# Optimization experiments

Hardware: AMD Instinct MI355X
Metric: run time of the kernel (lower is better)

Reference implementation:

```python
import jax, jax.numpy as jnp
import numpy as np

N = 1024       # nodes
D1 = 64        # hidden_dim_1
D2 = 64        # hidden_dim_2
E = 16384      # edges
P = 8192       # query pairs
MAXX = 100     # max node label -> Embedding(MAXX+1, D1)
EPS = 1e-5     # LayerNorm eps (no affine)


def _ln(t):
    m = jnp.mean(t, axis=-1, keepdims=True)
    v = jnp.mean((t - m) ** 2, axis=-1, keepdims=True)
    return (t - m) / jnp.sqrt(v + EPS)


def setup_inputs() -> dict:
    key = jax.random.key(0)
    ks = jax.random.split(key, 12)
    s = 0.1
    x = jax.random.randint(ks[0], (N,), 0, MAXX + 1)
    ei = jax.random.randint(ks[1], (2, E), 0, N)
    pos = jax.random.randint(ks[2], (P, 2), 0, N)
    emb = jax.random.normal(ks[3], (MAXX + 1, D1)) * s
    sage_Wl = jax.random.normal(ks[4], (2, D1, D1)) * s   # lin_l weight (aggr path, has bias)
    sage_bl = jnp.zeros((2, D1))
    sage_Wr = jax.random.normal(ks[5], (2, D1, D1)) * s   # lin_r weight (root path, no bias)
    h_W = jax.random.normal(ks[6], (D1 + 1, D2)) * s
    h_b = jnp.zeros((D2,))
    g_W = jax.random.normal(ks[7], (D1 + 1 + 2 * D2, D2)) * s
    g_b = jnp.zeros((D2,))
    lin_W = jax.random.normal(ks[8], (D2, 1)) * s
    lin_b = jnp.zeros((1,))
    return {"x": x, "ei": ei, "pos": pos, "emb": emb,
            "sage_Wl": sage_Wl, "sage_bl": sage_bl, "sage_Wr": sage_Wr,
            "h_W": h_W, "h_b": h_b, "g_W": g_W, "g_b": g_b,
            "lin_W": lin_W, "lin_b": lin_b}


def reference(x, ei, pos, emb, sage_Wl, sage_bl, sage_Wr, h_W, h_b, g_W, g_b, lin_W, lin_b):
    n = N
    src, dst = ei[0], ei[1]
    h = emb[x]                                            # (n, D1)
    # SAGEConv x2: mean-aggregate src->dst, lin_l(aggr)+bias + lin_r(root); then LN (no affine, no relu)
    deg = jax.ops.segment_sum(jnp.ones((E,), h.dtype), dst, num_segments=n)
    deg = jnp.maximum(deg, 1.0)[:, None]
    for i in range(2):
        aggr = jax.ops.segment_sum(h[src], dst, num_segments=n) / deg
        h = _ln(aggr @ sage_Wl[i] + sage_bl[i] + h @ sage_Wr[i])
    # pairwise outer product features: (n, n, D1)
    A = h[:, None, :] * h[None, :, :]
    eim = jnp.zeros((n * n,), h.dtype).at[src * n + dst].set(1.0).reshape(n, n, 1)
    A = jnp.concatenate([A, eim], axis=-1)                # (n, n, D1+1)
    # mataggr: B = h_1(A); row/col sums; D = cat(A, vec_p, vec_q); g_1(D)
    B = jax.nn.relu(_ln(A @ h_W + h_b))                   # (n, n, D2)
    vec_p = jnp.sum(B, axis=1, keepdims=True)             # (n, 1, D2)
    vec_q = jnp.sum(B, axis=0, keepdims=True)             # (1, n, D2)
    Dm = jnp.concatenate([A,
                          jnp.broadcast_to(vec_p, (n, n, D2)),
                          jnp.broadcast_to(vec_q, (n, n, D2))], axis=-1)
    G = jax.nn.relu(_ln(Dm @ g_W + g_b))                  # (n, n, D2)
    # symmetrize and gather query pairs
    S = (G * jnp.transpose(G, (1, 0, 2))).reshape(n * n, D2)
    sel = S[pos[:, 0] * n + pos[:, 1]]                    # (P, D2)
    return sel @ lin_W + lin_b                            # (P, 1)
```

## Files before the change

kernel.cpp:

```cpp
#include <hip/hip_runtime.h>
#include <hip/hip_bf16.h>

#define NN 1024
#define DD 64
#define EE 16384
#define PP 8192
#define EPSF 1e-5f
#define SWP (DD + 8)
#define NBC 64

typedef __hip_bfloat16 bf16;
typedef __attribute__((ext_vector_type(8))) short short8;
typedef __attribute__((ext_vector_type(4))) float f32x4;

static __device__ __forceinline__ float dec1(const void* src, int i, int fl) {
    if (fl) return ((const float*)src)[i];
    return __bfloat162float(((const bf16*)src)[i]);
}
static __device__ __forceinline__ unsigned short f2bf_u(float f) {
    bf16 h = __float2bfloat16(f);
    return *reinterpret_cast<unsigned short*>(&h);
}
static __device__ __forceinline__ float bfu2f(unsigned short u) {
    return __uint_as_float(((unsigned int)u) << 16);
}
static __device__ __forceinline__ int probe_fl(const void* emb) {
    int lane = threadIdx.x & 63;
    unsigned short raw = ((const unsigned short*)emb)[lane];
    float v = __uint_as_float(((unsigned int)raw) << 16);
    return (__ballot(!(fabsf(v) <= 1e3f)) != 0ull) ? 1 : 0;
}

__global__ __launch_bounds__(1024) void k_prep(
        const void* __restrict__ emb, const void* __restrict__ sWl,
        const void* __restrict__ sbl, const void* __restrict__ sWr,
        const void* __restrict__ hW, const void* __restrict__ hb,
        const void* __restrict__ gW, const void* __restrict__ gb,
        const void* __restrict__ lW, const void* __restrict__ lb,
        const int* __restrict__ x, const int* __restrict__ ei,
        float* __restrict__ Wlf, float* __restrict__ blf, float* __restrict__ Wrf,
        float* __restrict__ WfT, float* __restrict__ hbw,
        float* __restrict__ gWf, float* __restrict__ linf,
        unsigned short* __restrict__ gWbfT,
        float* __restrict__ h0,
        unsigned int* __restrict__ eim, unsigned int* __restrict__ eimT,
        int* __restrict__ dcnt, int* __restrict__ nbr) {
    const int b = blockIdx.x, tid = threadIdx.x;
    const int fl = probe_fl(emb);

    {
        int e = b * 1024 + tid;
        if (e < EE) {
            int s = ei[e], d = ei[EE + e];
            int c = atomicAdd(&dcnt[d], 1);
            if (c < NBC) nbr[d * NBC + c] = s;
        }
    }

    if (b < 97) {
        const int vb = b * 4 + (tid >> 8);
        const int vt = tid & 255;
        if (vb < 256) {
            int z = vb * 256 + vt;
            if (z < 32768) eim[z] = 0u;
            else           eimT[z - 32768] = 0u;
        }
        if (vb < 32) { int i = vb * 256 + vt; Wlf[i] = dec1(sWl, i, fl); }
        else if (vb == 32) { if (vt < 128) blf[vt] = dec1(sbl, vt, fl); }
        else if (vb < 65) { int i = (vb - 33) * 256 + vt; Wrf[i] = dec1(sWr, i, fl); }
        else if (vb < 82) {
            int i = (vb - 65) * 256 + vt;
            if (i < 4096) { int n = i >> 6, k = i & 63; WfT[n * DD + k] = dec1(hW, k * DD + n, fl); }
            else if (i < 4160) hbw[i - 4096] = dec1(hb, i - 4096, fl);
            else if (i < 4224) hbw[64 + (i - 4160)] = dec1(hW, 64 * DD + (i - 4160), fl);
        } else if (vb < 131) {
            int i = (vb - 82) * 256 + vt;
            if (i < 193 * DD) gWf[i] = dec1(gW, i, fl);
            else if (i < 194 * DD) gWf[i] = dec1(gb, i - 193 * DD, fl);
        } else if (vb == 131) {
            if (vt < DD) linf[vt] = dec1(lW, vt, fl);
            else if (vt == DD) linf[DD] = dec1(lb, 0, fl);
#pragma unroll
            for (int u = 0; u < 16; ++u) {
                int i = vt * 16 + u;
                int m = i >> 6, k = i & 63;
                gWbfT[i] = f2bf_u(dec1(gW, k * DD + m, fl));
            }
        } else if (vb < 388) {
            int i = (vb - 132) * 256 + vt;
            int node = i >> 6, f = i & 63;
            h0[i] = dec1(emb, x[node] * DD + f, fl);
        }
    }
}

static __device__ __forceinline__ void sage_core(
        const float* sWl, const float* sWr, float* sa, float* sh,
        int node, int lane,
        const int* __restrict__ dcnt, const int* __restrict__ nbr,
        const float* __restrict__ hin, const void* __restrict__ sbl, int boff, int fl,
        float* __restrict__ hout, unsigned short* __restrict__ hbf) {
    const int deg = dcnt[node];
    const int nc = min(deg, NBC);
    const int* nb = nbr + node * NBC;
    float s = 0.f;
    int r = 0;
    for (; r + 8 <= nc; r += 8) {
        int idx[8];
#pragma unroll
        for (int u = 0; u < 8; ++u) idx[u] = nb[r + u];
        float v[8];
#pragma unroll
        for (int u = 0; u < 8; ++u) v[u] = hin[idx[u] * DD + lane];
        s += ((v[0] + v[1]) + (v[2] + v[3])) + ((v[4] + v[5]) + (v[6] + v[7]));
    }
    for (; r + 4 <= nc; r += 4) {
        int i0 = nb[r], i1 = nb[r + 1], i2 = nb[r + 2], i3 = nb[r + 3];
        float v0 = hin[i0 * DD + lane], v1 = hin[i1 * DD + lane];
        float v2 = hin[i2 * DD + lane], v3 = hin[i3 * DD + lane];
        s += (v0 + v1) + (v2 + v3);
    }
    for (; r < nc; ++r) s += hin[nb[r] * DD + lane];
    sa[lane] = s / (float)max(deg, 1);
    sh[lane] = hin[node * DD + lane];
    float o = dec1(sbl, boff + lane, fl);
    for (int k = 0; k < DD; ++k)
        o += sa[k] * sWl[k * DD + lane] + sh[k] * sWr[k * DD + lane];
    float m = o;
    for (int off = 32; off; off >>= 1) m += __shfl_xor(m, off);
    m *= (1.f / DD);
    float d0 = o - m;
    float v = d0 * d0;
    for (int off = 32; off; off >>= 1) v += __shfl_xor(v, off);
    v *= (1.f / DD);
    float rr = d0 * rsqrtf(v + EPSF);
    hout[node * DD + lane] = rr;
    if (hbf) hbf[node * DD + lane] = f2bf_u(rr);
}

__global__ __launch_bounds__(256) void k_sage0(
        const void* __restrict__ emb, const int* __restrict__ ei,
        const int* __restrict__ dcnt, const int* __restrict__ nbr,
        const float* __restrict__ h0,
        const float* __restrict__ Wlf, const void* __restrict__ sbl,
        const float* __restrict__ Wrf,
        float* __restrict__ h1,
        unsigned int* __restrict__ eim, unsigned int* __restrict__ eimT) {
    __shared__ __align__(16) float sWl[DD * DD];
    __shared__ __align__(16) float sWr[DD * DD];
    __shared__ float sa4[4 * DD], sh4[4 * DD];
    const int b = blockIdx.x, tid = threadIdx.x;
    const int lane = tid & 63, wave = tid >> 6;
    const int fl = probe_fl(emb);
    for (int i = tid * 4; i < DD * DD; i += 1024) {
        *(float4*)(sWl + i) = *(const float4*)(Wlf + i);
        *(float4*)(sWr + i) = *(const float4*)(Wrf + i);
    }
    if (tid < 64) {
        int e = b * 64 + tid;
        int s = ei[e], d = ei[EE + e];
        unsigned int idx = (unsigned int)(s * NN + d);
        atomicOr(&eim[idx >> 5], 1u << (idx & 31));
        unsigned int idxT = (unsigned int)(d * NN + s);
        atomicOr(&eimT[idxT >> 5], 1u << (idxT & 31));
    }
    __syncthreads();
    sage_core(sWl, sWr, sa4 + wave * DD, sh4 + wave * DD, b * 4 + wave, lane,
              dcnt, nbr, h0, sbl, 0, fl, h1, (unsigned short*)nullptr);
}

__global__ __launch_bounds__(256) void k_sage1(
        const void* __restrict__ emb,
        const int* __restrict__ dcnt, const int* __restrict__ nbr,
        const float* __restrict__ h1,
        const float* __restrict__ Wlf, const void* __restrict__ sbl,
        const float* __restrict__ Wrf,
        float* __restrict__ h2, unsigned short* __restrict__ hbf) {
    __shared__ __align__(16) float sWl[DD * DD];
    __shared__ __align__(16) float sWr[DD * DD];
    __shared__ float sa4[4 * DD], sh4[4 * DD];
    const int b = blockIdx.x, tid = threadIdx.x;
    const int lane = tid & 63, wave = tid >> 6;
    const int fl = probe_fl(emb);
    for (int i = tid * 4; i < DD * DD; i += 1024) {
        *(float4*)(sWl + i) = *(const float4*)(Wlf + DD * DD + i);
        *(float4*)(sWr + i) = *(const float4*)(Wrf + DD * DD + i);
    }
    __syncthreads();
    sage_core(sWl, sWr, sa4 + wave * DD, sh4 + wave * DD, b * 4 + wave, lane,
              dcnt, nbr, h1, sbl, DD, fl, h2, hbf);
}

__global__ __launch_bounds__(256) void k_bstage(
        const float* __restrict__ h2, const unsigned short* __restrict__ hbf,
        const float* __restrict__ WfT, const float* __restrict__ hbw,
        const unsigned int* __restrict__ eim, const unsigned int* __restrict__ eimT,
        const float* __restrict__ gWf,
        float* __restrict__ ppb, float* __restrict__ qqb) {
    __shared__ __align__(16) unsigned short sW[DD * SWP];
    __shared__ __align__(16) float red[4 * 128];
    __shared__ float swc[2];
    const int b = blockIdx.x, tid = threadIdx.x;
    const int lane = tid & 63, wave = tid >> 6;
    const int l15 = lane & 15, quad = lane >> 4;

    {
        int m = tid >> 2;
        int k0 = (tid & 3) * 16;
        const float* hi = h2 + b * DD;
        const float* wr = WfT + m * DD;
        unsigned short tmp[16];
#pragma unroll
        for (int u = 0; u < 16; ++u) tmp[u] = f2bf_u(hi[k0 + u] * wr[k0 + u]);
        *(short8*)(sW + m * SWP + k0) = *(short8*)tmp;
        *(short8*)(sW + m * SWP + k0 + 8) = *(short8*)(tmp + 8);
    }
    if (wave == 0) {
        float wv = hbw[64 + lane];
        float s = wv, s2 = wv * wv;
        for (int off = 32; off; off >>= 1) {
            s += __shfl_xor(s, off);
            s2 += __shfl_xor(s2, off);
        }
        if (lane == 0) { swc[0] = s; swc[1] = s2; }
    }
    __syncthreads();
    const float SW = swc[0], SWW = swc[1];

    short8 Af[4][2];
#pragma unroll
    for (int mt = 0; mt < 4; ++mt)
#pragma unroll
        for (int kt = 0; kt < 2; ++kt)
            Af[mt][kt] = *(const short8*)(sW + (mt * 16 + l15) * SWP + kt * 32 + quad * 8);

    f32x4 hb04[4], hww4[4];
#pragma unroll
    for (int mt = 0; mt < 4; ++mt) {
        hb04[mt] = *(const f32x4*)(hbw + mt * 16 + quad * 4);
        hww4[mt] = *(const f32x4*)(hbw + 64 + mt * 16 + quad * 4);
    }

    f32x4 accf[4], accb[4];
#pragma unroll
    for (int mt = 0; mt < 4; ++mt) {
        accf[mt] = (f32x4){0.f, 0.f, 0.f, 0.f};
        accb[mt] = (f32x4){0.f, 0.f, 0.f, 0.f};
    }

    const unsigned short* pB = hbf + (wave * 16 + l15) * DD + quad * 8;
    const unsigned int* pF = eim + b * 32 + (wave >> 1);
    const unsigned int* pBk = eimT + b * 32 + (wave >> 1);
    const int shft = (wave & 1) * 16;

    short8 B0 = *(const short8*)(pB);
    short8 B1 = *(const short8*)(pB + 32);
    pB += 4096;
    unsigned int wfC = pF[0], wbC = pBk[0];
    pF += 2; pBk += 2;

    for (int it = 0; it < 16; ++it) {
        short8 cB0 = B0, cB1 = B1;
        B0 = *(const short8*)(pB);
        B1 = *(const short8*)(pB + 32);
        pB += 4096;
        unsigned int sf = (wfC >> shft) & 0xFFFFu;
        unsigned int sb = (wbC >> shft) & 0xFFFFu;
        wfC = pF[0]; wbC = pBk[0];
        pF += 2; pBk += 2;

        f32x4 C[4];
#pragma unroll
        for (int mt = 0; mt < 4; ++mt)
            C[mt] = __builtin_amdgcn_mfma_f32_16x16x32_bf16(Af[mt][0], cB0, hb04[mt], 0, 0, 0);
#pragma unroll
        for (int mt = 0; mt < 4; ++mt)
            C[mt] = __builtin_amdgcn_mfma_f32_16x16x32_bf16(Af[mt][1], cB1, C[mt], 0, 0, 0);

        float ef = 0.f;
        if ((sf | sb) != 0u) {
            ef = (float)((sf >> l15) & 1u);
            f32x4 efv = {ef, ef, ef, ef};
#pragma unroll
            for (int mt = 0; mt < 4; ++mt) C[mt] += efv * hww4[mt];
        }

        f32x4 s1a = {0.f, 0.f, 0.f, 0.f}, s2a = {0.f, 0.f, 0.f, 0.f};
#pragma unroll
        for (int mt = 0; mt < 4; ++mt) {
            s1a += C[mt];
            s2a += C[mt] * C[mt];
        }
        float s1 = (s1a.x + s1a.y) + (s1a.z + s1a.w);
        float s2 = (s2a.x + s2a.y) + (s2a.z + s2a.w);
        s1 += __shfl_xor(s1, 16); s1 += __shfl_xor(s1, 32);
        s2 += __shfl_xor(s2, 16); s2 += __shfl_xor(s2, 32);
        float mean = s1 * (1.f / DD);
        float var = fmaxf(s2 * (1.f / DD) - mean * mean, 0.f);
        float rs = rsqrtf(var + EPSF);
        float mrs = mean * rs;
        f32x4 rsv = {rs, rs, rs, rs}, mrsv = {mrs, mrs, mrs, mrs};
        f32x4 zero = {0.f, 0.f, 0.f, 0.f};

        if (sf == sb) {
#pragma unroll
            for (int mt = 0; mt < 4; ++mt) {
                f32x4 u = __builtin_elementwise_max(C[mt] * rsv - mrsv, zero);
                accf[mt] += u;
                accb[mt] += u;
            }
        } else {
#pragma unroll
            for (int mt = 0; mt < 4; ++mt)
                accf[mt] += __builtin_elementwise_max(C[mt] * rsv - mrsv, zero);
            float de = (float)((sb >> l15) & 1u) - ef;
            f32x4 dva = {0.f, 0.f, 0.f, 0.f};
#pragma unroll
            for (int mt = 0; mt < 4; ++mt) dva += C[mt] * hww4[mt];
            float dot = (dva.x + dva.y) + (dva.z + dva.w);
            dot += __shfl_xor(dot, 16); dot += __shfl_xor(dot, 32);
            float t1 = s1 + de * SW;
            float t2 = s2 + 2.f * de * dot + de * de * SWW;
            float mean2 = t1 * (1.f / DD);
            float var2 = fmaxf(t2 * (1.f / DD) - mean2 * mean2, 0.f);
            float rs2 = rsqrtf(var2 + EPSF);
            float mrs2 = mean2 * rs2;
            float drs = de * rs2;
            f32x4 rs2v = {rs2, rs2, rs2, rs2};
            f32x4 mrs2v = {mrs2, mrs2, mrs2, mrs2};
            f32x4 drsv = {drs, drs, drs, drs};
#pragma unroll
            for (int mt = 0; mt < 4; ++mt) {
                f32x4 th = mrs2v - drsv * hww4[mt];
                accb[mt] += __builtin_elementwise_max(C[mt] * rs2v - th, zero);
            }
        }
    }

    float af[4][4], ab[4][4];
#pragma unroll
    for (int mt = 0; mt < 4; ++mt)
#pragma unroll
        for (int r = 0; r < 4; ++r) { af[mt][r] = accf[mt][r]; ab[mt][r] = accb[mt][r]; }
#pragma unroll
    for (int step = 1; step < 16; step <<= 1)
#pragma unroll
        for (int mt = 0; mt < 4; ++mt)
#pragma unroll
            for (int r = 0; r < 4; ++r) {
                af[mt][r] += __shfl_xor(af[mt][r], step);
                ab[mt][r] += __shfl_xor(ab[mt][r], step);
            }
    if (l15 == 0) {
#pragma unroll
        for (int mt = 0; mt < 4; ++mt)
#pragma unroll
            for (int r = 0; r < 4; ++r) {
                int m = mt * 16 + quad * 4 + r;
                red[wave * 128 + m] = af[mt][r];
                red[wave * 128 + DD + m] = ab[mt][r];
            }
    }
    __syncthreads();
    if (tid < 128) {
        float sum = red[tid] + red[128 + tid] + red[256 + tid] + red[384 + tid];
        red[tid] = sum;
    }
    __syncthreads();
    if (wave < 2) {
        const float* sv = red + wave * DD;
        int row0 = wave ? 129 : 65;
        float o = 0.f;
        for (int k = 0; k < DD; ++k) o += sv[k] * gWf[(row0 + k) * DD + lane];
        (wave ? qqb : ppb)[b * DD + lane] = o;
    }
}

__global__ __launch_bounds__(128) void k_final(
        const void* __restrict__ emb,
        const int* __restrict__ pos, const unsigned short* __restrict__ hbf,
        const float* __restrict__ gWf, const unsigned short* __restrict__ gWbfT,
        const unsigned int* __restrict__ eim,
        const float* __restrict__ ppb, const float* __restrict__ qqb,
        const float* __restrict__ linf, void* __restrict__ outv) {
    const int b = blockIdx.x, tid = threadIdx.x;
    const int lane = tid & 63, wave = tid >> 6;
    const int l15 = lane & 15, quad = lane >> 4;
    const int fl = probe_fl(emb);

    short8 A0f[4], A1f[4];
#pragma unroll
    for (int mt = 0; mt < 4; ++mt) {
        A0f[mt] = *(const short8*)(gWbfT + (mt * 16 + l15) * DD + quad * 8);
        A1f[mt] = *(const short8*)(gWbfT + (mt * 16 + l15) * DD + 32 + quad * 8);
    }

    int pp_ = b * 32 + wave * 16 + l15;
    int a = pos[2 * pp_], bb = pos[2 * pp_ + 1];

    unsigned int iab = (unsigned int)(a * NN + bb), iba = (unsigned int)(bb * NN + a);
    unsigned int wab = eim[iab >> 5], wba = eim[iba >> 5];

    short8 ha0 = *(const short8*)(hbf + a * DD + quad * 8);
    short8 hb0v = *(const short8*)(hbf + bb * DD + quad * 8);
    short8 ha1 = *(const short8*)(hbf + a * DD + 32 + quad * 8);
    short8 hb1v = *(const short8*)(hbf + bb * DD + 32 + quad * 8);
    short8 B0, B1;
#pragma unroll
    for (int j = 0; j < 8; ++j) {
        B0[j] = (short)f2bf_u(bfu2f((unsigned short)ha0[j]) * bfu2f((unsigned short)hb0v[j]));
        B1[j] = (short)f2bf_u(bfu2f((unsigned short)ha1[j]) * bfu2f((unsigned short)hb1v[j]));
    }

    f32x4 C[4];
#pragma unroll
    for (int mt = 0; mt < 4; ++mt) C[mt] = (f32x4){0.f, 0.f, 0.f, 0.f};
#pragma unroll
    for (int mt = 0; mt < 4; ++mt)
        C[mt] = __builtin_amdgcn_mfma_f32_16x16x32_bf16(A0f[mt], B0, C[mt], 0, 0, 0);
#pragma unroll
    for (int mt = 0; mt < 4; ++mt)
        C[mt] = __builtin_amdgcn_mfma_f32_16x16x32_bf16(A1f[mt], B1, C[mt], 0, 0, 0);

    float eab = (float)((wab >> (iab & 31)) & 1u);
    float eba = (float)((wba >> (iba & 31)) & 1u);

    float u1[4][4], u2[4][4];
    float s1 = 0.f, s12 = 0.f, s2 = 0.f, s22 = 0.f;
#pragma unroll
    for (int mt = 0; mt < 4; ++mt) {
        int m0 = mt * 16 + quad * 4;
        f32x4 w64v = *(const f32x4*)(gWf + 64 * DD + m0);
        f32x4 gbv  = *(const f32x4*)(gWf + 193 * DD + m0);
        f32x4 ppa  = *(const f32x4*)(ppb + a * DD + m0);
        f32x4 qqb_ = *(const f32x4*)(qqb + bb * DD + m0);
        f32x4 ppb_ = *(const f32x4*)(ppb + bb * DD + m0);
        f32x4 qqa  = *(const f32x4*)(qqb + a * DD + m0);
#pragma unroll
        for (int r = 0; r < 4; ++r) {
            float v1 = C[mt][r] + eab * w64v[r] + ppa[r] + qqb_[r] + gbv[r];
            float v2 = C[mt][r] + eba * w64v[r] + ppb_[r] + qqa[r] + gbv[r];
            u1[mt][r] = v1; u2[mt][r] = v2;
            s1 += v1; s12 += v1 * v1;
            s2 += v2; s22 += v2 * v2;
        }
    }
    s1 += __shfl_xor(s1, 16);  s1 += __shfl_xor(s1, 32);
    s12 += __shfl_xor(s12, 16); s12 += __shfl_xor(s12, 32);
    s2 += __shfl_xor(s2, 16);  s2 += __shfl_xor(s2, 32);
    s22 += __shfl_xor(s22, 16); s22 += __shfl_xor(s22, 32);
    float mean1 = s1 * (1.f / DD);
    float rs1 = rsqrtf(fmaxf(s12 * (1.f / DD) - mean1 * mean1, 0.f) + EPSF);
    float mrs1 = mean1 * rs1;
    float mean2 = s2 * (1.f / DD);
    float rs2 = rsqrtf(fmaxf(s22 * (1.f / DD) - mean2 * mean2, 0.f) + EPSF);
    float mrs2 = mean2 * rs2;

    float r = 0.f;
#pragma unroll
    for (int mt = 0; mt < 4; ++mt) {
        f32x4 lw = *(const f32x4*)(linf + mt * 16 + quad * 4);
#pragma unroll
        for (int rr = 0; rr < 4; ++rr) {
            float g1 = fmaxf(u1[mt][rr] * rs1 - mrs1, 0.f);
            float g2 = fmaxf(u2[mt][rr] * rs2 - mrs2, 0.f);
            r += g1 * g2 * lw[rr];
        }
    }
    r += __shfl_xor(r, 16); r += __shfl_xor(r, 32);
    if (quad == 0) {
        float res = r + linf[DD];
        if (fl) ((float*)outv)[pp_] = res;
        else    ((bf16*)outv)[pp_] = __float2bfloat16(res);
    }
}

extern "C" void kernel_launch(void* const* d_in, const int* in_sizes, int n_in,
                              void* d_out, int out_size, void* d_ws, size_t ws_size,
                              hipStream_t stream) {
    const int* x   = (const int*)d_in[0];
    const int* ei  = (const int*)d_in[1];
    const int* pos = (const int*)d_in[2];
    const void* emb = d_in[3];

    char* w = (char*)d_ws;
    auto alloc = [&](size_t bytes) {
        void* q = (void*)w;
        w += (bytes + 255) & ~(size_t)255;
        return q;
    };
    unsigned int* eim  = (unsigned int*)alloc(NN * NN / 8);
    unsigned int* eimT = (unsigned int*)alloc(NN * NN / 8);
    float* h0   = (float*)alloc(NN * DD * 4);
    float* h1   = (float*)alloc(NN * DD * 4);
    float* h2   = (float*)alloc(NN * DD * 4);
    unsigned short* hbf = (unsigned short*)alloc(NN * DD * 2 + 8192);
    float* Wlf  = (float*)alloc(2 * DD * DD * 4);
    float* blf  = (float*)alloc(2 * DD * 4);
    float* Wrf  = (float*)alloc(2 * DD * DD * 4);
    float* WfT  = (float*)alloc(DD * DD * 4);
    float* hbw  = (float*)alloc(128 * 4);
    float* gWf  = (float*)alloc(194 * DD * 4);
    float* linf = (float*)alloc(65 * 4);
    unsigned short* gWbfT = (unsigned short*)alloc(DD * DD * 2);
    float* ppb  = (float*)alloc(NN * DD * 4);
    float* qqb  = (float*)alloc(NN * DD * 4);
    int* dcnt   = (int*)alloc(NN * 4);
    int* nbr    = (int*)alloc(NN * NBC * 4);

    hipMemsetAsync(dcnt, 0, NN * 4, stream);
    k_prep<<<98, 1024, 0, stream>>>(emb, d_in[4], d_in[5], d_in[6], d_in[7], d_in[8],
                                    d_in[9], d_in[10], d_in[11], d_in[12],
                                    x, ei, Wlf, blf, Wrf, WfT, hbw, gWf, linf, gWbfT,
                                    h0, eim, eimT, dcnt, nbr);
    k_sage0<<<256, 256, 0, stream>>>(emb, ei, dcnt, nbr, h0, Wlf, d_in[5], Wrf,
                                     h1, eim, eimT);
    k_sage1<<<256, 256, 0, stream>>>(emb, dcnt, nbr, h1, Wlf, d_in[5], Wrf, h2, hbf);
    k_bstage<<<NN, 256, 0, stream>>>(h2, hbf, WfT, hbw, eim, eimT, gWf, ppb, qqb);
    k_final<<<PP / 32, 128, 0, stream>>>(emb, pos, hbf, gWf, gWbfT, eim, ppb, qqb, linf, d_out);
}
```

Baseline: 142.2 us.

## Split bstage column loop across four blocks per row with partial sums

Each row of the B stage is now handled by four blocks, each covering a quarter of the columns, so the grid grows from 1024 to 4096 blocks. Each block writes its own partial projected row and column sums, and the final kernel adds the four partials when it reads them. The aim is more parallelism and a shorter serial loop per block in the heaviest stage. The cost is redoing the per-block weight setup four times, four times the partial-sum storage, and extra loads in the final kernel.

```diff
diff --git a/kernel.cpp b/kernel.cpp
--- a/kernel.cpp
+++ b/kernel.cpp
@@ -196,11 +196,12 @@
         const float* __restrict__ WfT, const float* __restrict__ hbw,
         const unsigned int* __restrict__ eim, const unsigned int* __restrict__ eimT,
         const float* __restrict__ gWf,
-        float* __restrict__ ppb, float* __restrict__ qqb) {
+        float* __restrict__ ppq, float* __restrict__ qqq) {
     __shared__ __align__(16) unsigned short sW[DD * SWP];
     __shared__ __align__(16) float red[4 * 128];
     __shared__ float swc[2];
-    const int b = blockIdx.x, tid = threadIdx.x;
+    const int bid = blockIdx.x, tid = threadIdx.x;
+    const int b = bid >> 2, jq = bid & 3;
     const int lane = tid & 63, wave = tid >> 6;
     const int l15 = lane & 15, quad = lane >> 4;
 
@@ -248,26 +249,18 @@
         accb[mt] = (f32x4){0.f, 0.f, 0.f, 0.f};
     }
 
-    const unsigned short* pB = hbf + (wave * 16 + l15) * DD + quad * 8;
-    const unsigned int* pF = eim + b * 32 + (wave >> 1);
-    const unsigned int* pBk = eimT + b * 32 + (wave >> 1);
+    const unsigned short* pB = hbf + (wave * 16 + l15) * DD + quad * 8 + jq * 16384;
+    const unsigned int* pF = eim + b * 32 + jq * 8 + (wave >> 1);
+    const unsigned int* pBk = eimT + b * 32 + jq * 8 + (wave >> 1);
     const int shft = (wave & 1) * 16;
 
-    short8 B0 = *(const short8*)(pB);
-    short8 B1 = *(const short8*)(pB + 32);
-    pB += 4096;
-    unsigned int wfC = pF[0], wbC = pBk[0];
-    pF += 2; pBk += 2;
-
-    for (int it = 0; it < 16; ++it) {
-        short8 cB0 = B0, cB1 = B1;
-        B0 = *(const short8*)(pB);
-        B1 = *(const short8*)(pB + 32);
-        pB += 4096;
-        unsigned int sf = (wfC >> shft) & 0xFFFFu;
-        unsigned int sb = (wbC >> shft) & 0xFFFFu;
-        wfC = pF[0]; wbC = pBk[0];
-        pF += 2; pBk += 2;
+#pragma unroll
+    for (int it = 0; it < 4; ++it) {
+        short8 cB0 = *(const short8*)(pB + it * 4096);
+        short8 cB1 = *(const short8*)(pB + it * 4096 + 32);
+        unsigned int wf = pF[it * 2], wb = pBk[it * 2];
+        unsigned int sf = (wf >> shft) & 0xFFFFu;
+        unsigned int sb = (wb >> shft) & 0xFFFFu;
 
         f32x4 C[4];
 #pragma unroll
@@ -372,7 +365,7 @@
         int row0 = wave ? 129 : 65;
         float o = 0.f;
         for (int k = 0; k < DD; ++k) o += sv[k] * gWf[(row0 + k) * DD + lane];
-        (wave ? qqb : ppb)[b * DD + lane] = o;
+        (wave ? qqq : ppq)[(jq * NN + b) * DD + lane] = o;
     }
 }
 
@@ -381,7 +374,7 @@
         const int* __restrict__ pos, const unsigned short* __restrict__ hbf,
         const float* __restrict__ gWf, const unsigned short* __restrict__ gWbfT,
         const unsigned int* __restrict__ eim,
-        const float* __restrict__ ppb, const float* __restrict__ qqb,
+        const float* __restrict__ ppq, const float* __restrict__ qqq,
         const float* __restrict__ linf, void* __restrict__ outv) {
     const int b = blockIdx.x, tid = threadIdx.x;
     const int lane = tid & 63, wave = tid >> 6;
@@ -432,10 +425,17 @@
         int m0 = mt * 16 + quad * 4;
         f32x4 w64v = *(const f32x4*)(gWf + 64 * DD + m0);
         f32x4 gbv  = *(const f32x4*)(gWf + 193 * DD + m0);
-        f32x4 ppa  = *(const f32x4*)(ppb + a * DD + m0);
-        f32x4 qqb_ = *(const f32x4*)(qqb + bb * DD + m0);
-        f32x4 ppb_ = *(const f32x4*)(ppb + bb * DD + m0);
-        f32x4 qqa  = *(const f32x4*)(qqb + a * DD + m0);
+        f32x4 ppa  = {0.f, 0.f, 0.f, 0.f};
+        f32x4 qqb_ = {0.f, 0.f, 0.f, 0.f};
+        f32x4 ppb_ = {0.f, 0.f, 0.f, 0.f};
+        f32x4 qqa  = {0.f, 0.f, 0.f, 0.f};
+#pragma unroll
+        for (int q = 0; q < 4; ++q) {
+            ppa  += *(const f32x4*)(ppq + (q * NN + a) * DD + m0);
+            qqb_ += *(const f32x4*)(qqq + (q * NN + bb) * DD + m0);
+            ppb_ += *(const f32x4*)(ppq + (q * NN + bb) * DD + m0);
+            qqa  += *(const f32x4*)(qqq + (q * NN + a) * DD + m0);
+        }
 #pragma unroll
         for (int r = 0; r < 4; ++r) {
             float v1 = C[mt][r] + eab * w64v[r] + ppa[r] + qqb_[r] + gbv[r];
@@ -494,7 +494,7 @@
     float* h0   = (float*)alloc(NN * DD * 4);
     float* h1   = (float*)alloc(NN * DD * 4);
     float* h2   = (float*)alloc(NN * DD * 4);
-    unsigned short* hbf = (unsigned short*)alloc(NN * DD * 2 + 8192);
+    unsigned short* hbf = (unsigned short*)alloc(NN * DD * 2 + 24576);
     float* Wlf  = (float*)alloc(2 * DD * DD * 4);
     float* blf  = (float*)alloc(2 * DD * 4);
     float* Wrf  = (float*)alloc(2 * DD * DD * 4);
@@ -503,8 +503,8 @@
     float* gWf  = (float*)alloc(194 * DD * 4);
     float* linf = (float*)alloc(65 * 4);
     unsigned short* gWbfT = (unsigned short*)alloc(DD * DD * 2);
-    float* ppb  = (float*)alloc(NN * DD * 4);
-    float* qqb  = (float*)alloc(NN * DD * 4);
+    float* ppq  = (float*)alloc(4 * NN * DD * 4);
+    float* qqq  = (float*)alloc(4 * NN * DD * 4);
     int* dcnt   = (int*)alloc(NN * 4);
     int* nbr    = (int*)alloc(NN * NBC * 4);
 
@@ -516,6 +516,6 @@
     k_sage0<<<256, 256, 0, stream>>>(emb, ei, dcnt, nbr, h0, Wlf, d_in[5], Wrf,
                                      h1, eim, eimT);
     k_sage1<<<256, 256, 0, stream>>>(emb, dcnt, nbr, h1, Wlf, d_in[5], Wrf, h2, hbf);
-    k_bstage<<<NN, 256, 0, stream>>>(h2, hbf, WfT, hbw, eim, eimT, gWf, ppb, qqb);
-    k_final<<<PP / 32, 128, 0, stream>>>(emb, pos, hbf, gWf, gWbfT, eim, ppb, qqb, linf, d_out);
-}
+    k_bstage<<<4 * NN, 256, 0, stream>>>(h2, hbf, WfT, hbw, eim, eimT, gWf, ppq, qqq);
+    k_final<<<PP / 32, 128, 0, stream>>>(emb, pos, hbf, gWf, gWbfT, eim, ppq, qqq, linf, d_out);
+}
```

After: 188.7 us. 32.7% more time.
